# Kernel tuning notes

Hardware: AMD Instinct MI355X
Metric: run time of the kernel (lower is better)

## Reference

```python
import jax, jax.numpy as jnp
import numpy as np

N_NODES = 65536
N_EDGES = 524288
N_GRAPHS = 64
PTS_PER_GRAPH = 1024


def gcn_conv(x, W, b, row, col, self_idx, n_nodes):
    # PyG GCNConv: x' = D^{-1/2} (A + I) D^{-1/2} x W + b
    xw = x @ W
    row2 = jnp.concatenate([row, self_idx])
    col2 = jnp.concatenate([col, self_idx])
    deg = jax.ops.segment_sum(jnp.ones_like(col2, dtype=xw.dtype), col2, num_segments=n_nodes)
    dinv = jax.lax.rsqrt(deg)  # deg >= 1 thanks to self-loops
    norm = dinv[row2] * dinv[col2]  # [E+N]
    out = jax.ops.segment_sum(xw[row2] * norm[:, None], col2, num_segments=n_nodes)
    return out + b


def setup_inputs() -> dict:
    key = jax.random.key(0)
    ks = jax.random.split(key, 12)

    def glorot(k, fan_in, fan_out):
        s = jnp.sqrt(6.0 / (fan_in + fan_out))
        return jax.random.uniform(k, (fan_in, fan_out), jnp.float32, -s, s)

    x = jax.random.normal(ks[0], (N_NODES, 3), jnp.float32)
    edge_index = jax.random.randint(ks[1], (2, N_EDGES), 0, N_NODES, dtype=jnp.int64)
    batch = (jnp.arange(N_NODES, dtype=jnp.int64) // PTS_PER_GRAPH)  # 64 graphs x 1024 pts

    return {
        "x": x, "edge_index": edge_index, "batch": batch,
        "W1": glorot(ks[2], 3, 64), "b1": jnp.zeros((64,), jnp.float32),
        "W2": glorot(ks[3], 64, 256), "b2": jnp.zeros((256,), jnp.float32),
        "W3": glorot(ks[4], 256, 512), "b3": jnp.zeros((512,), jnp.float32),
        "Wm1": glorot(ks[5], 1024, 512), "bm1": jnp.zeros((512,), jnp.float32),
        "Wm2": glorot(ks[6], 512, 10), "bm2": jnp.zeros((10,), jnp.float32),
    }


def reference(x, edge_index, batch, W1, b1, W2, b2, W3, b3, Wm1, bm1, Wm2, bm2):
    n = x.shape[0]
    row, col = edge_index[0], edge_index[1]
    self_idx = jnp.arange(n, dtype=edge_index.dtype)

    x1 = jax.nn.relu(gcn_conv(x, W1, b1, row, col, self_idx, n))
    x2 = jax.nn.relu(gcn_conv(x1, W2, b2, row, col, self_idx, n))
    x3 = jax.nn.relu(gcn_conv(x2, W3, b3, row, col, self_idx, n))

    # global mean / max pool over batch segments
    counts = jax.ops.segment_sum(jnp.ones((n,), x3.dtype), batch, num_segments=N_GRAPHS)
    x_mean = jax.ops.segment_sum(x3, batch, num_segments=N_GRAPHS) / counts[:, None]
    x_max = jax.ops.segment_max(x3, batch, num_segments=N_GRAPHS)
    h = jnp.concatenate([x_mean, x_max], axis=1)  # [G, 1024]

    h = jax.nn.relu(h @ Wm1 + bm1)  # dropout is identity in eval
    return h @ Wm2 + bm2  # [G, 10]
```

## Files before the change

### kernel.cpp

```cpp
#include <hip/hip_runtime.h>
#include <hip/hip_bf16.h>

typedef __hip_bfloat16 bf16;
typedef short bf16x8 __attribute__((ext_vector_type(8)));
typedef float f32x4 __attribute__((ext_vector_type(4)));

__device__ __forceinline__ float b2f_us(unsigned short u) {
    union { unsigned int i; float f; } c;
    c.i = ((unsigned int)u) << 16;
    return c.f;
}
__device__ __forceinline__ unsigned short f2b_us(float f) {
    bf16 h = __float2bfloat16(f);
    return *reinterpret_cast<unsigned short*>(&h);
}
__device__ __forceinline__ void unpack8(uint4 p, float* f) {
    f[0] = b2f_us(p.x & 0xffff); f[1] = b2f_us(p.x >> 16);
    f[2] = b2f_us(p.y & 0xffff); f[3] = b2f_us(p.y >> 16);
    f[4] = b2f_us(p.z & 0xffff); f[5] = b2f_us(p.z >> 16);
    f[6] = b2f_us(p.w & 0xffff); f[7] = b2f_us(p.w >> 16);
}

__device__ __forceinline__ void async_copy16(const bf16* g, bf16* l) {
    __builtin_amdgcn_global_load_lds(
        (const __attribute__((address_space(1))) unsigned int*)g,
        (__attribute__((address_space(3))) unsigned int*)l, 16, 0, 0);
}

__global__ __launch_bounds__(256) void k_count(const int* __restrict__ col,
                                               int* __restrict__ cnt, int E) {
    int e = blockIdx.x * 256 + threadIdx.x;
    if (e < E) atomicAdd(cnt + col[e], 1);
}
__global__ __launch_bounds__(256) void k_rsqrt(const int* __restrict__ cnt,
                                               float* __restrict__ dinv, int N) {
    int i = blockIdx.x * 256 + threadIdx.x;
    if (i < N) dinv[i] = rsqrtf((float)cnt[i] + 1.0f);
}

__global__ __launch_bounds__(256) void k_scan_a(const int* __restrict__ cnt,
                                                int* __restrict__ bsum) {
    __shared__ int s[256];
    int t = threadIdx.x;
    s[t] = cnt[blockIdx.x * 256 + t];
    __syncthreads();
#pragma unroll
    for (int off = 128; off >= 1; off >>= 1) {
        if (t < off) s[t] += s[t + off];
        __syncthreads();
    }
    if (t == 0) bsum[blockIdx.x] = s[0];
}
__global__ __launch_bounds__(256) void k_scan_b(const int* __restrict__ bsum,
                                                int* __restrict__ boff) {
    __shared__ int s[256];
    int t = threadIdx.x;
    int self = bsum[t];
    s[t] = self;
    __syncthreads();
#pragma unroll
    for (int off = 1; off < 256; off <<= 1) {
        int v = (t >= off) ? s[t - off] : 0;
        __syncthreads();
        s[t] += v;
        __syncthreads();
    }
    boff[t] = s[t] - self;
}
__global__ __launch_bounds__(256) void k_scan_c(const int* __restrict__ cnt,
                                                const int* __restrict__ boff,
                                                int* __restrict__ rowptr) {
    __shared__ int s[256];
    int t = threadIdx.x;
    int base = blockIdx.x * 256;
    int self = cnt[base + t];
    s[t] = self;
    __syncthreads();
#pragma unroll
    for (int off = 1; off < 256; off <<= 1) {
        int v = (t >= off) ? s[t - off] : 0;
        __syncthreads();
        s[t] += v;
        __syncthreads();
    }
    rowptr[base + t] = boff[blockIdx.x] + s[t] - self;
}

__global__ __launch_bounds__(256) void k_scatter(const int* __restrict__ row,
                                                 const int* __restrict__ col,
                                                 const float* __restrict__ dinv,
                                                 const int* __restrict__ rowptr,
                                                 int* __restrict__ fill,
                                                 int2* __restrict__ adj, int E) {
    int e = blockIdx.x * 256 + threadIdx.x;
    if (e >= E) return;
    int r = row[e], c = col[e];
    int pos = rowptr[c] + atomicAdd(fill + c, 1);
    adj[pos] = make_int2(r, __float_as_int(dinv[r]));
}

__global__ __launch_bounds__(256) void k_prep(const float* __restrict__ W,
                                              bf16* __restrict__ WT, int K, int N) {
    int idx = blockIdx.x * 256 + threadIdx.x;
    if (idx >= K * N) return;
    int k = idx / N, n = idx - k * N;
    WT[(size_t)n * K + k] = __float2bfloat16(W[idx]);
}

__global__ __launch_bounds__(256) void k_gather_x(const int2* __restrict__ adj,
                                                  const int* __restrict__ rowptr,
                                                  const int* __restrict__ cnt,
                                                  const float* __restrict__ dinv,
                                                  const float* __restrict__ x,
                                                  float* __restrict__ agg1, int N) {
    int n = blockIdx.x * 256 + threadIdx.x;
    if (n >= N) return;
    float d = dinv[n];
    float d2 = d * d;
    float a0 = x[n * 3] * d2, a1 = x[n * 3 + 1] * d2, a2 = x[n * 3 + 2] * d2;
    int beg = rowptr[n], end = beg + cnt[n];
    for (int e = beg; e < end; ++e) {
        int2 ad = adj[e];
        float w = __int_as_float(ad.y) * d;
        a0 += x[ad.x * 3] * w;
        a1 += x[ad.x * 3 + 1] * w;
        a2 += x[ad.x * 3 + 2] * w;
    }
    agg1[n * 3] = a0; agg1[n * 3 + 1] = a1; agg1[n * 3 + 2] = a2;
}

__global__ __launch_bounds__(256) void k_gemm1(const float* __restrict__ agg1,
                                               const float* __restrict__ W,
                                               const float* __restrict__ bias,
                                               bf16* __restrict__ h1, int M) {
    __shared__ float w[256];
    int t = threadIdx.x;
    if (t < 192) w[t] = W[t];
    if (t >= 192) w[t] = bias[t - 192];
    __syncthreads();
    int idx = blockIdx.x * 256 + t;
    if (idx < M * 64) {
        int n = idx >> 6, f = idx & 63;
        float acc = agg1[n * 3] * w[f] + agg1[n * 3 + 1] * w[64 + f] +
                    agg1[n * 3 + 2] * w[128 + f] + w[192 + f];
        h1[idx] = __float2bfloat16(fmaxf(acc, 0.f));
    }
}

template <int F>
__global__ __launch_bounds__(256) void k_gather_pre(const int2* __restrict__ adj,
                                                    const int* __restrict__ rowptr,
                                                    const int* __restrict__ cnt,
                                                    const float* __restrict__ dinv,
                                                    const bf16* __restrict__ h,
                                                    bf16* __restrict__ agg, int N) {
    constexpr int LPN = F / 8;
    constexpr int NPB = 256 / LPN;
    int t = threadIdx.x;
    int node = blockIdx.x * NPB + t / LPN;
    if (node >= N) return;
    int fbase = (t % LPN) * 8;
    float d = dinv[node];
    size_t sbase = (size_t)node * F + fbase;
    uint4 sp = *reinterpret_cast<const uint4*>(h + sbase);
    float a[8];
    unpack8(sp, a);
    float d2 = d * d;
#pragma unroll
    for (int i = 0; i < 8; i++) a[i] *= d2;
    int beg = rowptr[node];
    int end = beg + cnt[node];
    int e = beg;
    for (; e + 3 < end; e += 4) {
        int2 ad0 = adj[e], ad1 = adj[e + 1], ad2 = adj[e + 2], ad3 = adj[e + 3];
        const uint4 p0 = *reinterpret_cast<const uint4*>(h + (size_t)ad0.x * F + fbase);
        const uint4 p1 = *reinterpret_cast<const uint4*>(h + (size_t)ad1.x * F + fbase);
        const uint4 p2 = *reinterpret_cast<const uint4*>(h + (size_t)ad2.x * F + fbase);
        const uint4 p3 = *reinterpret_cast<const uint4*>(h + (size_t)ad3.x * F + fbase);
        float w0 = __int_as_float(ad0.y) * d;
        float w1 = __int_as_float(ad1.y) * d;
        float w2 = __int_as_float(ad2.y) * d;
        float w3 = __int_as_float(ad3.y) * d;
        float f0[8], f1[8], f2[8], f3[8];
        unpack8(p0, f0); unpack8(p1, f1); unpack8(p2, f2); unpack8(p3, f3);
#pragma unroll
        for (int i = 0; i < 8; i++)
            a[i] += f0[i] * w0 + f1[i] * w1 + f2[i] * w2 + f3[i] * w3;
    }
    for (; e < end; ++e) {
        int2 ad = adj[e];
        float w = __int_as_float(ad.y) * d;
        uint4 p = *reinterpret_cast<const uint4*>(h + (size_t)ad.x * F + fbase);
        float f[8];
        unpack8(p, f);
#pragma unroll
        for (int i = 0; i < 8; i++) a[i] += f[i] * w;
    }
    uint4 r;
    r.x = (unsigned)f2b_us(a[0]) | ((unsigned)f2b_us(a[1]) << 16);
    r.y = (unsigned)f2b_us(a[2]) | ((unsigned)f2b_us(a[3]) << 16);
    r.z = (unsigned)f2b_us(a[4]) | ((unsigned)f2b_us(a[5]) << 16);
    r.w = (unsigned)f2b_us(a[6]) | ((unsigned)f2b_us(a[7]) << 16);
    *reinterpret_cast<uint4*>(agg + sbase) = r;
}

__global__ __launch_bounds__(256) void k_gemm_br(const bf16* __restrict__ A,
                                                 const bf16* __restrict__ BT,
                                                 const float* __restrict__ bias,
                                                 bf16* __restrict__ C,
                                                 int M, int N, int K) {
    __shared__ bf16 As[128 * 32];
    __shared__ bf16 Bs[128 * 32];
    const int t = threadIdx.x;
    const int wave = t >> 6, lane = t & 63;
    const int quad = lane >> 4, l16 = lane & 15;
    const int wm = wave & 1, wn = wave >> 1;
    const int m0 = blockIdx.x * 128;
    const int n0 = blockIdx.y * 128;

    f32x4 acc[4][4] = {};
    for (int kb = 0; kb < K; kb += 32) {
#pragma unroll
        for (int rnd = 0; rnd < 2; ++rnd) {
            int c = (rnd * 4 + wave) * 64 + lane;
            int r = c >> 2, seg = c & 3;
            async_copy16(A + (size_t)(m0 + r) * K + kb + seg * 8, As + c * 8);
            async_copy16(BT + (size_t)(n0 + r) * K + kb + seg * 8, Bs + c * 8);
        }
        __syncthreads();
        bf16x8 af[4], bfr[4];
#pragma unroll
        for (int i = 0; i < 4; i++)
            af[i] = *reinterpret_cast<const bf16x8*>(&As[(wm * 64 + i * 16 + l16) * 32 + quad * 8]);
#pragma unroll
        for (int j = 0; j < 4; j++)
            bfr[j] = *reinterpret_cast<const bf16x8*>(&Bs[(wn * 64 + j * 16 + l16) * 32 + quad * 8]);
#pragma unroll
        for (int i = 0; i < 4; i++)
#pragma unroll
            for (int j = 0; j < 4; j++)
                acc[i][j] = __builtin_amdgcn_mfma_f32_16x16x32_bf16(af[i], bfr[j], acc[i][j], 0, 0, 0);
        __syncthreads();
    }
#pragma unroll
    for (int j = 0; j < 4; j++) {
        int cn = n0 + wn * 64 + j * 16 + l16;
        float bv = bias[cn];
#pragma unroll
        for (int i = 0; i < 4; i++) {
            int row = m0 + wm * 64 + i * 16 + quad * 4;
#pragma unroll
            for (int r = 0; r < 4; r++)
                C[(size_t)(row + r) * N + cn] = __float2bfloat16(fmaxf(acc[i][j][r] + bv, 0.f));
        }
    }
}

__global__ __launch_bounds__(256) void k_gemm_pool(const bf16* __restrict__ A,
                                                   const bf16* __restrict__ BT,
                                                   const float* __restrict__ bias,
                                                   float* __restrict__ partials,
                                                   int M, int N, int K) {
    __shared__ bf16 As[128 * 32];
    __shared__ bf16 Bs[128 * 32];
    const int t = threadIdx.x;
    const int wave = t >> 6, lane = t & 63;
    const int quad = lane >> 4, l16 = lane & 15;
    const int wm = wave & 1, wn = wave >> 1;
    const int m0 = blockIdx.x * 128;
    const int n0 = blockIdx.y * 128;

    f32x4 acc[4][4] = {};
    for (int kb = 0; kb < K; kb += 32) {
#pragma unroll
        for (int rnd = 0; rnd < 2; ++rnd) {
            int c = (rnd * 4 + wave) * 64 + lane;
            int r = c >> 2, seg = c & 3;
            async_copy16(A + (size_t)(m0 + r) * K + kb + seg * 8, As + c * 8);
            async_copy16(BT + (size_t)(n0 + r) * K + kb + seg * 8, Bs + c * 8);
        }
        __syncthreads();
        bf16x8 af[4], bfr[4];
#pragma unroll
        for (int i = 0; i < 4; i++)
            af[i] = *reinterpret_cast<const bf16x8*>(&As[(wm * 64 + i * 16 + l16) * 32 + quad * 8]);
#pragma unroll
        for (int j = 0; j < 4; j++)
            bfr[j] = *reinterpret_cast<const bf16x8*>(&Bs[(wn * 64 + j * 16 + l16) * 32 + quad * 8]);
#pragma unroll
        for (int i = 0; i < 4; i++)
#pragma unroll
            for (int j = 0; j < 4; j++)
                acc[i][j] = __builtin_amdgcn_mfma_f32_16x16x32_bf16(af[i], bfr[j], acc[i][j], 0, 0, 0);
        __syncthreads();
    }
    size_t pbase = ((size_t)(blockIdx.x * 4 + blockIdx.y) * 2 + wm) * 256;
#pragma unroll
    for (int j = 0; j < 4; j++) {
        int f128 = wn * 64 + j * 16 + l16;
        float bv = bias[n0 + f128];
        float s = 0.f, mx = 0.f;
#pragma unroll
        for (int i = 0; i < 4; i++)
#pragma unroll
            for (int r = 0; r < 4; r++) {
                float v = fmaxf(acc[i][j][r] + bv, 0.f);
                s += v;
                mx = fmaxf(mx, v);
            }
        s += __shfl_xor(s, 16);
        s += __shfl_xor(s, 32);
        mx = fmaxf(mx, __shfl_xor(mx, 16));
        mx = fmaxf(mx, __shfl_xor(mx, 32));
        if (quad == 0) {
            partials[pbase + f128] = s;
            partials[pbase + 128 + f128] = mx;
        }
    }
}

__global__ __launch_bounds__(256) void k_pool_final(const float* __restrict__ partials,
                                                    float* __restrict__ pooled) {
    int idx = blockIdx.x * 256 + threadIdx.x;
    int g = idx >> 9, f = idx & 511;
    int by = f >> 7, f128 = f & 127;
    float S = 0.f, M = 0.f;
#pragma unroll
    for (int tile = 0; tile < 8; ++tile) {
        int bx = g * 8 + tile;
#pragma unroll
        for (int wm = 0; wm < 2; ++wm) {
            size_t pbase = ((size_t)(bx * 4 + by) * 2 + wm) * 256;
            S += partials[pbase + f128];
            M = fmaxf(M, partials[pbase + 128 + f128]);
        }
    }
    pooled[g * 1024 + f] = S * (1.0f / 1024.0f);
    pooled[g * 1024 + 512 + f] = M;
}

__global__ __launch_bounds__(256) void k_mlp1(const float* __restrict__ pooled,
                                              const float* __restrict__ Wm1,
                                              const float* __restrict__ bm1,
                                              float* __restrict__ o) {
    __shared__ float hg[1024];
    __shared__ float red[256];
    int g = blockIdx.x;
    int t = threadIdx.x;
    int f64 = t & 63, kq = t >> 6;
    int f = blockIdx.y * 64 + f64;
#pragma unroll
    for (int i = 0; i < 4; i++) hg[t + i * 256] = pooled[g * 1024 + t + i * 256];
    __syncthreads();
    float acc = 0.f;
    int k0 = kq * 256;
#pragma unroll 8
    for (int k = k0; k < k0 + 256; ++k)
        acc += hg[k] * Wm1[(size_t)k * 512 + f];
    red[t] = acc;
    __syncthreads();
    if (t < 64) {
        float total = red[t] + red[t + 64] + red[t + 128] + red[t + 192] + bm1[f];
        o[g * 512 + f] = fmaxf(total, 0.f);
    }
}

__global__ __launch_bounds__(512) void k_mlp2(const float* __restrict__ h,
                                              const float* __restrict__ Wm2,
                                              const float* __restrict__ bm2,
                                              float* __restrict__ out) {
    int g = blockIdx.x;
    int t = threadIdx.x;
    int j = t >> 5, lane32 = t & 31;
    float acc = 0.f;
    if (j < 10) {
        int k0 = lane32 * 16;
#pragma unroll
        for (int i = 0; i < 16; ++i)
            acc += h[g * 512 + k0 + i] * Wm2[(size_t)(k0 + i) * 10 + j];
    }
#pragma unroll
    for (int m = 16; m >= 1; m >>= 1) acc += __shfl_xor(acc, m);
    if (j < 10 && lane32 == 0) out[g * 10 + j] = acc + bm2[j];
}

extern "C" void kernel_launch(void* const* d_in, const int* in_sizes, int n_in,
                              void* d_out, int out_size, void* d_ws, size_t ws_size,
                              hipStream_t stream) {
    const float* x   = (const float*)d_in[0];
    const int*   ei  = (const int*)d_in[1];
    const float* W1  = (const float*)d_in[3];
    const float* b1  = (const float*)d_in[4];
    const float* W2  = (const float*)d_in[5];
    const float* b2  = (const float*)d_in[6];
    const float* W3  = (const float*)d_in[7];
    const float* b3  = (const float*)d_in[8];
    const float* Wm1 = (const float*)d_in[9];
    const float* bm1 = (const float*)d_in[10];
    const float* Wm2 = (const float*)d_in[11];
    const float* bm2 = (const float*)d_in[12];
    float* out = (float*)d_out;

    const int N = in_sizes[0] / 3;
    const int E = in_sizes[1] / 2;
    const int* row = ei;
    const int* col = ei + E;

    char* ws = (char*)d_ws;
    size_t off = 0;
    auto alloc = [&](size_t bytes) {
        void* p = ws + off;
        off += (bytes + 255) & ~(size_t)255;
        return p;
    };
    int*   cnt      = (int*)alloc((size_t)N * 4);
    int*   rowptr   = (int*)alloc((size_t)N * 4);
    int*   fill     = (int*)alloc((size_t)N * 4);
    float* dinv     = (float*)alloc((size_t)N * 4);
    int*   bsum     = (int*)alloc(256 * 4);
    int*   boff     = (int*)alloc(256 * 4);
    int2*  adj      = (int2*)alloc((size_t)E * 8);
    float* agg1     = (float*)alloc((size_t)N * 3 * 4);
    bf16*  h1       = (bf16*)alloc((size_t)N * 64 * 2);
    bf16*  agg2     = (bf16*)alloc((size_t)N * 64 * 2);
    bf16*  h2       = (bf16*)alloc((size_t)N * 256 * 2);
    bf16*  agg3     = (bf16*)alloc((size_t)N * 256 * 2);
    bf16*  WT2      = (bf16*)alloc(256 * 64 * 2);
    bf16*  WT3      = (bf16*)alloc(512 * 256 * 2);
    float* partials = (float*)alloc((size_t)512 * 4 * 2 * 256 * 4);
    float* pooled   = (float*)alloc(64 * 1024 * 4);
    float* m1       = (float*)alloc(64 * 512 * 4);

    hipMemsetAsync(cnt, 0, (size_t)N * 4, stream);
    hipMemsetAsync(fill, 0, (size_t)N * 4, stream);
    k_count<<<(E + 255) / 256, 256, 0, stream>>>(col, cnt, E);
    k_rsqrt<<<(N + 255) / 256, 256, 0, stream>>>(cnt, dinv, N);
    k_scan_a<<<256, 256, 0, stream>>>(cnt, bsum);
    k_scan_b<<<1, 256, 0, stream>>>(bsum, boff);
    k_scan_c<<<256, 256, 0, stream>>>(cnt, boff, rowptr);
    k_scatter<<<(E + 255) / 256, 256, 0, stream>>>(row, col, dinv, rowptr, fill, adj, E);

    k_prep<<<(64 * 256 + 255) / 256, 256, 0, stream>>>(W2, WT2, 64, 256);
    k_prep<<<(256 * 512 + 255) / 256, 256, 0, stream>>>(W3, WT3, 256, 512);

    k_gather_x<<<(N + 255) / 256, 256, 0, stream>>>(adj, rowptr, cnt, dinv, x, agg1, N);
    k_gemm1<<<(N * 64) / 256, 256, 0, stream>>>(agg1, W1, b1, h1, N);

    k_gather_pre<64><<<(N * 8) / 256, 256, 0, stream>>>(adj, rowptr, cnt, dinv, h1, agg2, N);
    k_gemm_br<<<dim3(N / 128, 256 / 128), 256, 0, stream>>>(agg2, WT2, b2, h2, N, 256, 64);

    k_gather_pre<256><<<(N * 32) / 256, 256, 0, stream>>>(adj, rowptr, cnt, dinv, h2, agg3, N);
    k_gemm_pool<<<dim3(N / 128, 512 / 128), 256, 0, stream>>>(agg3, WT3, b3, partials, N, 512, 256);
    k_pool_final<<<(64 * 512) / 256, 256, 0, stream>>>(partials, pooled);

    k_mlp1<<<dim3(64, 8), 256, 0, stream>>>(pooled, Wm1, bm1, m1);
    k_mlp2<<<64, 512, 0, stream>>>(m1, Wm2, bm2, out);
}
```

Before: 284.9 us.

## Fuse layer-3 neighbor gather into the pooled GEMM kernel via LDS staging

Replaces the separate layer-3 gather kernel and the GEMM+pool kernel with one kernel. Each block aggregates 64 nodes' neighbor features into LDS as bf16, then loops over all four 128-wide output column tiles, running MFMA and reducing sum/max partials. This removes the N x 256 bf16 agg3 round trip through global memory and one launch. In exchange, each thread gathers with 64 fp32 accumulators, which raises register pressure, and the gather is serialized per thread over irregular degrees, so occupancy and latency hiding may suffer.

```diff
diff --git a/kernel.cpp b/kernel.cpp
--- a/kernel.cpp
+++ b/kernel.cpp
@@ -256,65 +256,115 @@
     }
 }
 
-__global__ __launch_bounds__(256) void k_gemm_pool(const bf16* __restrict__ A,
-                                                   const bf16* __restrict__ BT,
-                                                   const float* __restrict__ bias,
-                                                   float* __restrict__ partials,
-                                                   int M, int N, int K) {
-    __shared__ bf16 As[128 * 32];
+__global__ __launch_bounds__(256) void k_gcn3(const int2* __restrict__ adj,
+                                              const int* __restrict__ rowptr,
+                                              const int* __restrict__ cnt,
+                                              const float* __restrict__ dinv,
+                                              const bf16* __restrict__ h2,
+                                              const bf16* __restrict__ BT,
+                                              const float* __restrict__ bias,
+                                              float* __restrict__ partials) {
+    __shared__ bf16 As[8][64][32];
     __shared__ bf16 Bs[128 * 32];
     const int t = threadIdx.x;
+    const int m0 = blockIdx.x * 64;
+
+    {
+        int row = t >> 2, q = t & 3;
+        int fbase = q * 64;
+        int node = m0 + row;
+        float d = dinv[node];
+        float d2 = d * d;
+        float a[64];
+        const bf16* hrow = h2 + (size_t)node * 256 + fbase;
+#pragma unroll
+        for (int i = 0; i < 8; i++) {
+            uint4 p = *reinterpret_cast<const uint4*>(hrow + i * 8);
+            float f[8];
+            unpack8(p, f);
+#pragma unroll
+            for (int j = 0; j < 8; j++) a[i * 8 + j] = f[j] * d2;
+        }
+        int beg = rowptr[node], end = beg + cnt[node];
+        for (int e = beg; e < end; ++e) {
+            int2 ad = adj[e];
+            float w = __int_as_float(ad.y) * d;
+            const bf16* src = h2 + (size_t)ad.x * 256 + fbase;
+            uint4 p[8];
+#pragma unroll
+            for (int i = 0; i < 8; i++)
+                p[i] = *reinterpret_cast<const uint4*>(src + i * 8);
+#pragma unroll
+            for (int i = 0; i < 8; i++) {
+                float f[8];
+                unpack8(p[i], f);
+#pragma unroll
+                for (int j = 0; j < 8; j++) a[i * 8 + j] += f[j] * w;
+            }
+        }
+#pragma unroll
+        for (int i = 0; i < 8; i++) {
+            int f = fbase + i * 8;
+            int c = f >> 5, off = f & 31;
+            uint4 r;
+            r.x = (unsigned)f2b_us(a[i * 8 + 0]) | ((unsigned)f2b_us(a[i * 8 + 1]) << 16);
+            r.y = (unsigned)f2b_us(a[i * 8 + 2]) | ((unsigned)f2b_us(a[i * 8 + 3]) << 16);
+            r.z = (unsigned)f2b_us(a[i * 8 + 4]) | ((unsigned)f2b_us(a[i * 8 + 5]) << 16);
+            r.w = (unsigned)f2b_us(a[i * 8 + 6]) | ((unsigned)f2b_us(a[i * 8 + 7]) << 16);
+            *reinterpret_cast<uint4*>(&As[c][row][off]) = r;
+        }
+    }
+    __syncthreads();
+
     const int wave = t >> 6, lane = t & 63;
     const int quad = lane >> 4, l16 = lane & 15;
-    const int wm = wave & 1, wn = wave >> 1;
-    const int m0 = blockIdx.x * 128;
-    const int n0 = blockIdx.y * 128;
-
-    f32x4 acc[4][4] = {};
-    for (int kb = 0; kb < K; kb += 32) {
-#pragma unroll
-        for (int rnd = 0; rnd < 2; ++rnd) {
-            int c = (rnd * 4 + wave) * 64 + lane;
-            int r = c >> 2, seg = c & 3;
-            async_copy16(A + (size_t)(m0 + r) * K + kb + seg * 8, As + c * 8);
-            async_copy16(BT + (size_t)(n0 + r) * K + kb + seg * 8, Bs + c * 8);
-        }
-        __syncthreads();
-        bf16x8 af[4], bfr[4];
-#pragma unroll
-        for (int i = 0; i < 4; i++)
-            af[i] = *reinterpret_cast<const bf16x8*>(&As[(wm * 64 + i * 16 + l16) * 32 + quad * 8]);
-#pragma unroll
-        for (int j = 0; j < 4; j++)
-            bfr[j] = *reinterpret_cast<const bf16x8*>(&Bs[(wn * 64 + j * 16 + l16) * 32 + quad * 8]);
-#pragma unroll
-        for (int i = 0; i < 4; i++)
-#pragma unroll
-            for (int j = 0; j < 4; j++)
-                acc[i][j] = __builtin_amdgcn_mfma_f32_16x16x32_bf16(af[i], bfr[j], acc[i][j], 0, 0, 0);
-        __syncthreads();
-    }
-    size_t pbase = ((size_t)(blockIdx.x * 4 + blockIdx.y) * 2 + wm) * 256;
-#pragma unroll
-    for (int j = 0; j < 4; j++) {
-        int f128 = wn * 64 + j * 16 + l16;
-        float bv = bias[n0 + f128];
-        float s = 0.f, mx = 0.f;
-#pragma unroll
-        for (int i = 0; i < 4; i++)
-#pragma unroll
-            for (int r = 0; r < 4; r++) {
-                float v = fmaxf(acc[i][j][r] + bv, 0.f);
-                s += v;
-                mx = fmaxf(mx, v);
+    for (int nt = 0; nt < 4; ++nt) {
+        f32x4 acc[4][2] = {};
+        for (int kc = 0; kc < 8; ++kc) {
+#pragma unroll
+            for (int rnd = 0; rnd < 2; ++rnd) {
+                int c = (rnd * 4 + wave) * 64 + lane;
+                int r = c >> 2, seg = c & 3;
+                async_copy16(BT + (size_t)(nt * 128 + r) * 256 + kc * 32 + seg * 8,
+                             Bs + c * 8);
             }
-        s += __shfl_xor(s, 16);
-        s += __shfl_xor(s, 32);
-        mx = fmaxf(mx, __shfl_xor(mx, 16));
-        mx = fmaxf(mx, __shfl_xor(mx, 32));
-        if (quad == 0) {
-            partials[pbase + f128] = s;
-            partials[pbase + 128 + f128] = mx;
+            __syncthreads();
+            bf16x8 af[4], bfr[2];
+#pragma unroll
+            for (int i = 0; i < 4; i++)
+                af[i] = *reinterpret_cast<const bf16x8*>(&As[kc][i * 16 + l16][quad * 8]);
+#pragma unroll
+            for (int j = 0; j < 2; j++)
+                bfr[j] = *reinterpret_cast<const bf16x8*>(&Bs[(wave * 32 + j * 16 + l16) * 32 + quad * 8]);
+#pragma unroll
+            for (int i = 0; i < 4; i++)
+#pragma unroll
+                for (int j = 0; j < 2; j++)
+                    acc[i][j] = __builtin_amdgcn_mfma_f32_16x16x32_bf16(af[i], bfr[j], acc[i][j], 0, 0, 0);
+            __syncthreads();
+        }
+        size_t pbase = ((size_t)blockIdx.x * 4 + nt) * 256;
+#pragma unroll
+        for (int j = 0; j < 2; j++) {
+            int f128 = wave * 32 + j * 16 + l16;
+            float bv = bias[nt * 128 + f128];
+            float s = 0.f, mx = 0.f;
+#pragma unroll
+            for (int i = 0; i < 4; i++)
+#pragma unroll
+                for (int r = 0; r < 4; r++) {
+                    float v = fmaxf(acc[i][j][r] + bv, 0.f);
+                    s += v;
+                    mx = fmaxf(mx, v);
+                }
+            s += __shfl_xor(s, 16);
+            s += __shfl_xor(s, 32);
+            mx = fmaxf(mx, __shfl_xor(mx, 16));
+            mx = fmaxf(mx, __shfl_xor(mx, 32));
+            if (quad == 0) {
+                partials[pbase + f128] = s;
+                partials[pbase + 128 + f128] = mx;
+            }
         }
     }
 }
@@ -326,14 +376,10 @@
     int by = f >> 7, f128 = f & 127;
     float S = 0.f, M = 0.f;
 #pragma unroll
-    for (int tile = 0; tile < 8; ++tile) {
-        int bx = g * 8 + tile;
-#pragma unroll
-        for (int wm = 0; wm < 2; ++wm) {
-            size_t pbase = ((size_t)(bx * 4 + by) * 2 + wm) * 256;
-            S += partials[pbase + f128];
-            M = fmaxf(M, partials[pbase + 128 + f128]);
-        }
+    for (int tile = 0; tile < 16; ++tile) {
+        size_t pbase = ((size_t)(g * 16 + tile) * 4 + by) * 256;
+        S += partials[pbase + f128];
+        M = fmaxf(M, partials[pbase + 128 + f128]);
     }
     pooled[g * 1024 + f] = S * (1.0f / 1024.0f);
     pooled[g * 1024 + 512 + f] = M;
@@ -424,10 +470,9 @@
     bf16*  h1       = (bf16*)alloc((size_t)N * 64 * 2);
     bf16*  agg2     = (bf16*)alloc((size_t)N * 64 * 2);
     bf16*  h2       = (bf16*)alloc((size_t)N * 256 * 2);
-    bf16*  agg3     = (bf16*)alloc((size_t)N * 256 * 2);
     bf16*  WT2      = (bf16*)alloc(256 * 64 * 2);
     bf16*  WT3      = (bf16*)alloc(512 * 256 * 2);
-    float* partials = (float*)alloc((size_t)512 * 4 * 2 * 256 * 4);
+    float* partials = (float*)alloc((size_t)1024 * 4 * 256 * 4);
     float* pooled   = (float*)alloc(64 * 1024 * 4);
     float* m1       = (float*)alloc(64 * 512 * 4);
 
@@ -449,8 +494,7 @@
     k_gather_pre<64><<<(N * 8) / 256, 256, 0, stream>>>(adj, rowptr, cnt, dinv, h1, agg2, N);
     k_gemm_br<<<dim3(N / 128, 256 / 128), 256, 0, stream>>>(agg2, WT2, b2, h2, N, 256, 64);
 
-    k_gather_pre<256><<<(N * 32) / 256, 256, 0, stream>>>(adj, rowptr, cnt, dinv, h2, agg3, N);
-    k_gemm_pool<<<dim3(N / 128, 512 / 128), 256, 0, stream>>>(agg3, WT3, b3, partials, N, 512, 256);
+    k_gcn3<<<N / 64, 256, 0, stream>>>(adj, rowptr, cnt, dinv, h2, WT3, b3, partials);
     k_pool_final<<<(64 * 512) / 256, 256, 0, stream>>>(partials, pooled);
 
     k_mlp1<<<dim3(64, 8), 256, 0, stream>>>(pooled, Wm1, bm1, m1);
```

Result: slower. 302.1 us (+6.0%).

## Fuse small setup kernels, merge layer-1 gather with GEMM, deepen gather unroll

Applied to the files above, without the earlier changes.

Folds the rsqrt degree computation into the first scan kernel and merges the two weight-transpose kernels into one launch. The layer-1 gather and its tiny 3x64 GEMM become one kernel, so the agg1 round trip is gone. The two memsets become one by making cnt and fill adjacent. The bf16 gather loop now issues 8 independent neighbour loads per iteration with a min-occupancy hint, to expose more memory parallelism. This removes several launches at the cost of more registers per thread, and k_gcn1 now does wide per-thread stores of 64 outputs per node.

```diff
diff --git a/kernel.cpp b/kernel.cpp
--- a/kernel.cpp
+++ b/kernel.cpp
@@ -32,17 +32,15 @@
     int e = blockIdx.x * 256 + threadIdx.x;
     if (e < E) atomicAdd(cnt + col[e], 1);
 }
-__global__ __launch_bounds__(256) void k_rsqrt(const int* __restrict__ cnt,
-                                               float* __restrict__ dinv, int N) {
-    int i = blockIdx.x * 256 + threadIdx.x;
-    if (i < N) dinv[i] = rsqrtf((float)cnt[i] + 1.0f);
-}
-
 __global__ __launch_bounds__(256) void k_scan_a(const int* __restrict__ cnt,
-                                                int* __restrict__ bsum) {
+                                                int* __restrict__ bsum,
+                                                float* __restrict__ dinv) {
     __shared__ int s[256];
     int t = threadIdx.x;
-    s[t] = cnt[blockIdx.x * 256 + t];
+    int i = blockIdx.x * 256 + t;
+    int c = cnt[i];
+    dinv[i] = rsqrtf((float)c + 1.0f);
+    s[t] = c;
     __syncthreads();
 #pragma unroll
     for (int off = 128; off >= 1; off >>= 1) {
@@ -99,21 +97,37 @@
     adj[pos] = make_int2(r, __float_as_int(dinv[r]));
 }
 
-__global__ __launch_bounds__(256) void k_prep(const float* __restrict__ W,
-                                              bf16* __restrict__ WT, int K, int N) {
+__global__ __launch_bounds__(256) void k_prep_all(const float* __restrict__ W2,
+                                                  bf16* __restrict__ WT2,
+                                                  const float* __restrict__ W3,
+                                                  bf16* __restrict__ WT3) {
     int idx = blockIdx.x * 256 + threadIdx.x;
-    if (idx >= K * N) return;
-    int k = idx / N, n = idx - k * N;
-    WT[(size_t)n * K + k] = __float2bfloat16(W[idx]);
-}
-
-__global__ __launch_bounds__(256) void k_gather_x(const int2* __restrict__ adj,
-                                                  const int* __restrict__ rowptr,
-                                                  const int* __restrict__ cnt,
-                                                  const float* __restrict__ dinv,
-                                                  const float* __restrict__ x,
-                                                  float* __restrict__ agg1, int N) {
-    int n = blockIdx.x * 256 + threadIdx.x;
+    if (idx < 64 * 256) {
+        int k = idx >> 8, n = idx & 255;
+        WT2[n * 64 + k] = __float2bfloat16(W2[idx]);
+    } else {
+        int i = idx - 64 * 256;
+        if (i < 256 * 512) {
+            int k = i >> 9, n = i & 511;
+            WT3[(size_t)n * 256 + k] = __float2bfloat16(W3[i]);
+        }
+    }
+}
+
+__global__ __launch_bounds__(256) void k_gcn1(const int2* __restrict__ adj,
+                                              const int* __restrict__ rowptr,
+                                              const int* __restrict__ cnt,
+                                              const float* __restrict__ dinv,
+                                              const float* __restrict__ x,
+                                              const float* __restrict__ W,
+                                              const float* __restrict__ bias,
+                                              bf16* __restrict__ h1, int N) {
+    __shared__ float w[256];
+    int t = threadIdx.x;
+    if (t < 192) w[t] = W[t];
+    else w[t] = bias[t - 192];
+    __syncthreads();
+    int n = blockIdx.x * 256 + t;
     if (n >= N) return;
     float d = dinv[n];
     float d2 = d * d;
@@ -121,39 +135,36 @@
     int beg = rowptr[n], end = beg + cnt[n];
     for (int e = beg; e < end; ++e) {
         int2 ad = adj[e];
-        float w = __int_as_float(ad.y) * d;
-        a0 += x[ad.x * 3] * w;
-        a1 += x[ad.x * 3 + 1] * w;
-        a2 += x[ad.x * 3 + 2] * w;
-    }
-    agg1[n * 3] = a0; agg1[n * 3 + 1] = a1; agg1[n * 3 + 2] = a2;
-}
-
-__global__ __launch_bounds__(256) void k_gemm1(const float* __restrict__ agg1,
-                                               const float* __restrict__ W,
-                                               const float* __restrict__ bias,
-                                               bf16* __restrict__ h1, int M) {
-    __shared__ float w[256];
-    int t = threadIdx.x;
-    if (t < 192) w[t] = W[t];
-    if (t >= 192) w[t] = bias[t - 192];
-    __syncthreads();
-    int idx = blockIdx.x * 256 + t;
-    if (idx < M * 64) {
-        int n = idx >> 6, f = idx & 63;
-        float acc = agg1[n * 3] * w[f] + agg1[n * 3 + 1] * w[64 + f] +
-                    agg1[n * 3 + 2] * w[128 + f] + w[192 + f];
-        h1[idx] = __float2bfloat16(fmaxf(acc, 0.f));
+        float wt = __int_as_float(ad.y) * d;
+        a0 += x[ad.x * 3] * wt;
+        a1 += x[ad.x * 3 + 1] * wt;
+        a2 += x[ad.x * 3 + 2] * wt;
+    }
+    bf16* dst = h1 + (size_t)n * 64;
+#pragma unroll
+    for (int fb = 0; fb < 8; ++fb) {
+        uint4 r;
+        unsigned v[4];
+#pragma unroll
+        for (int p = 0; p < 4; ++p) {
+            int f0 = fb * 8 + p * 2;
+            float u0 = fmaxf(a0 * w[f0] + a1 * w[64 + f0] + a2 * w[128 + f0] + w[192 + f0], 0.f);
+            int f1 = f0 + 1;
+            float u1 = fmaxf(a0 * w[f1] + a1 * w[64 + f1] + a2 * w[128 + f1] + w[192 + f1], 0.f);
+            v[p] = (unsigned)f2b_us(u0) | ((unsigned)f2b_us(u1) << 16);
+        }
+        r.x = v[0]; r.y = v[1]; r.z = v[2]; r.w = v[3];
+        *reinterpret_cast<uint4*>(dst + fb * 8) = r;
     }
 }
 
 template <int F>
-__global__ __launch_bounds__(256) void k_gather_pre(const int2* __restrict__ adj,
-                                                    const int* __restrict__ rowptr,
-                                                    const int* __restrict__ cnt,
-                                                    const float* __restrict__ dinv,
-                                                    const bf16* __restrict__ h,
-                                                    bf16* __restrict__ agg, int N) {
+__global__ __launch_bounds__(256, 4) void k_gather_pre(const int2* __restrict__ adj,
+                                                       const int* __restrict__ rowptr,
+                                                       const int* __restrict__ cnt,
+                                                       const float* __restrict__ dinv,
+                                                       const bf16* __restrict__ h,
+                                                       bf16* __restrict__ agg, int N) {
     constexpr int LPN = F / 8;
     constexpr int NPB = 256 / LPN;
     int t = threadIdx.x;
@@ -171,30 +182,48 @@
     int beg = rowptr[node];
     int end = beg + cnt[node];
     int e = beg;
+    for (; e + 7 < end; e += 8) {
+        int2 ad[8];
+        uint4 p[8];
+#pragma unroll
+        for (int u = 0; u < 8; ++u) ad[u] = adj[e + u];
+#pragma unroll
+        for (int u = 0; u < 8; ++u)
+            p[u] = *reinterpret_cast<const uint4*>(h + (size_t)ad[u].x * F + fbase);
+#pragma unroll
+        for (int u = 0; u < 8; ++u) {
+            float wt = __int_as_float(ad[u].y) * d;
+            float f[8];
+            unpack8(p[u], f);
+#pragma unroll
+            for (int i = 0; i < 8; i++) a[i] += f[i] * wt;
+        }
+    }
     for (; e + 3 < end; e += 4) {
-        int2 ad0 = adj[e], ad1 = adj[e + 1], ad2 = adj[e + 2], ad3 = adj[e + 3];
-        const uint4 p0 = *reinterpret_cast<const uint4*>(h + (size_t)ad0.x * F + fbase);
-        const uint4 p1 = *reinterpret_cast<const uint4*>(h + (size_t)ad1.x * F + fbase);
-        const uint4 p2 = *reinterpret_cast<const uint4*>(h + (size_t)ad2.x * F + fbase);
-        const uint4 p3 = *reinterpret_cast<const uint4*>(h + (size_t)ad3.x * F + fbase);
-        float w0 = __int_as_float(ad0.y) * d;
-        float w1 = __int_as_float(ad1.y) * d;
-        float w2 = __int_as_float(ad2.y) * d;
-        float w3 = __int_as_float(ad3.y) * d;
-        float f0[8], f1[8], f2[8], f3[8];
-        unpack8(p0, f0); unpack8(p1, f1); unpack8(p2, f2); unpack8(p3, f3);
-#pragma unroll
-        for (int i = 0; i < 8; i++)
-            a[i] += f0[i] * w0 + f1[i] * w1 + f2[i] * w2 + f3[i] * w3;
+        int2 ad[4];
+        uint4 p[4];
+#pragma unroll
+        for (int u = 0; u < 4; ++u) ad[u] = adj[e + u];
+#pragma unroll
+        for (int u = 0; u < 4; ++u)
+            p[u] = *reinterpret_cast<const uint4*>(h + (size_t)ad[u].x * F + fbase);
+#pragma unroll
+        for (int u = 0; u < 4; ++u) {
+            float wt = __int_as_float(ad[u].y) * d;
+            float f[8];
+            unpack8(p[u], f);
+#pragma unroll
+            for (int i = 0; i < 8; i++) a[i] += f[i] * wt;
+        }
     }
     for (; e < end; ++e) {
         int2 ad = adj[e];
-        float w = __int_as_float(ad.y) * d;
+        float wt = __int_as_float(ad.y) * d;
         uint4 p = *reinterpret_cast<const uint4*>(h + (size_t)ad.x * F + fbase);
         float f[8];
         unpack8(p, f);
 #pragma unroll
-        for (int i = 0; i < 8; i++) a[i] += f[i] * w;
+        for (int i = 0; i < 8; i++) a[i] += f[i] * wt;
     }
     uint4 r;
     r.x = (unsigned)f2b_us(a[0]) | ((unsigned)f2b_us(a[1]) << 16);
@@ -414,13 +443,12 @@
         return p;
     };
     int*   cnt      = (int*)alloc((size_t)N * 4);
+    int*   fill     = (int*)alloc((size_t)N * 4);
     int*   rowptr   = (int*)alloc((size_t)N * 4);
-    int*   fill     = (int*)alloc((size_t)N * 4);
     float* dinv     = (float*)alloc((size_t)N * 4);
     int*   bsum     = (int*)alloc(256 * 4);
     int*   boff     = (int*)alloc(256 * 4);
     int2*  adj      = (int2*)alloc((size_t)E * 8);
-    float* agg1     = (float*)alloc((size_t)N * 3 * 4);
     bf16*  h1       = (bf16*)alloc((size_t)N * 64 * 2);
     bf16*  agg2     = (bf16*)alloc((size_t)N * 64 * 2);
     bf16*  h2       = (bf16*)alloc((size_t)N * 256 * 2);
@@ -431,20 +459,16 @@
     float* pooled   = (float*)alloc(64 * 1024 * 4);
     float* m1       = (float*)alloc(64 * 512 * 4);
 
-    hipMemsetAsync(cnt, 0, (size_t)N * 4, stream);
-    hipMemsetAsync(fill, 0, (size_t)N * 4, stream);
+    hipMemsetAsync(cnt, 0, (size_t)N * 8, stream);
     k_count<<<(E + 255) / 256, 256, 0, stream>>>(col, cnt, E);
-    k_rsqrt<<<(N + 255) / 256, 256, 0, stream>>>(cnt, dinv, N);
-    k_scan_a<<<256, 256, 0, stream>>>(cnt, bsum);
+    k_scan_a<<<256, 256, 0, stream>>>(cnt, bsum, dinv);
     k_scan_b<<<1, 256, 0, stream>>>(bsum, boff);
     k_scan_c<<<256, 256, 0, stream>>>(cnt, boff, rowptr);
     k_scatter<<<(E + 255) / 256, 256, 0, stream>>>(row, col, dinv, rowptr, fill, adj, E);
 
-    k_prep<<<(64 * 256 + 255) / 256, 256, 0, stream>>>(W2, WT2, 64, 256);
-    k_prep<<<(256 * 512 + 255) / 256, 256, 0, stream>>>(W3, WT3, 256, 512);
-
-    k_gather_x<<<(N + 255) / 256, 256, 0, stream>>>(adj, rowptr, cnt, dinv, x, agg1, N);
-    k_gemm1<<<(N * 64) / 256, 256, 0, stream>>>(agg1, W1, b1, h1, N);
+    k_prep_all<<<(64 * 256 + 256 * 512 + 255) / 256, 256, 0, stream>>>(W2, WT2, W3, WT3);
+
+    k_gcn1<<<(N + 255) / 256, 256, 0, stream>>>(adj, rowptr, cnt, dinv, x, W1, b1, h1, N);
 
     k_gather_pre<64><<<(N * 8) / 256, 256, 0, stream>>>(adj, rowptr, cnt, dinv, h1, agg2, N);
     k_gemm_br<<<dim3(N / 128, 256 / 128), 256, 0, stream>>>(agg2, WT2, b2, h2, N, 256, 64);
```

New measurement: 274.7 us (median of 2 runs). 1.04x faster.
